# Performance work log

Hardware: AMD Instinct MI355X
Metric: run time of the kernel (lower is better)

Reference implementation:

```python
import jax, jax.numpy as jnp
import numpy as np

D_HEAD = 64
D_MODEL = 1024
N_HEADS = D_MODEL // D_HEAD
MAX_TOKENS = 2048


def setup_inputs() -> dict:
    key = jax.random.key(0)
    ks = jax.random.split(key, 5)
    batch, pos = 2, 2048
    # kaiming_normal_ on (n_heads, d_model, d_head): fan_in = d_model*d_head -> std = sqrt(2/fan_in)
    std_qkv = np.sqrt(2.0 / (D_MODEL * D_HEAD)).astype(np.float32)
    # xavier_normal_ on (d_model, d_model): std = sqrt(2/(fan_in+fan_out))
    std_out = np.sqrt(2.0 / (D_MODEL + D_MODEL)).astype(np.float32)
    return {
        "residual_stream": jax.random.normal(ks[0], (batch, pos, D_MODEL), dtype=jnp.float32),
        "weight_query": jax.random.normal(ks[1], (N_HEADS, D_MODEL, D_HEAD), dtype=jnp.float32) * std_qkv,
        "weight_key": jax.random.normal(ks[2], (N_HEADS, D_MODEL, D_HEAD), dtype=jnp.float32) * std_qkv,
        "weight_value": jax.random.normal(ks[3], (N_HEADS, D_MODEL, D_HEAD), dtype=jnp.float32) * std_qkv,
        "weight_out": jax.random.normal(ks[4], (D_MODEL, D_MODEL), dtype=jnp.float32) * std_out,
    }


def reference(residual_stream, weight_query, weight_key, weight_value, weight_out):
    # QKV projections: [b, p, m] x [h, m, d] -> [b, h, p, d]
    q = jnp.einsum('bpm,hmd->bhpd', residual_stream, weight_query)
    k = jnp.einsum('bpm,hmd->bhpd', residual_stream, weight_key)
    v = jnp.einsum('bpm,hmd->bhpd', residual_stream, weight_value)

    n_tokens = residual_stream.shape[1]
    # scaled scores [b, h, dest, src]
    scores = jnp.einsum('bhqd,bhkd->bhqk', q, k) / jnp.sqrt(jnp.float32(D_HEAD))
    # causal mask: -inf above the diagonal
    causal = jnp.tril(jnp.ones((n_tokens, n_tokens), dtype=bool))
    scores = jnp.where(causal, scores, jnp.float32(-jnp.inf))
    pattern = jax.nn.softmax(scores, axis=-1)

    attn = jnp.einsum('bhqk,bhkd->bhqd', pattern, v)  # [b, h, dest, d_head]
    # concat heads -> [b, p, h*d_head]
    b, h, p, d = attn.shape
    attn_concat = jnp.transpose(attn, (0, 2, 1, 3)).reshape(b, p, h * d)
    return jnp.einsum('bpm,mn->bpn', attn_concat, weight_out)
```

## Files before the change

kernel.cpp:

```cpp
#include <hip/hip_runtime.h>
#include <hip/hip_bf16.h>
#include <stdint.h>


typedef __bf16 bf16x8 __attribute__((ext_vector_type(8)));
typedef float f32x4 __attribute__((ext_vector_type(4)));
typedef float f32x16 __attribute__((ext_vector_type(16)));
typedef unsigned short u16;

__device__ __forceinline__ u16 f2bf(float f) {
  unsigned u = __float_as_uint(f);
  u += 0x7fffu + ((u >> 16) & 1u);
  return (u16)(u >> 16);
}

__device__ __forceinline__ uint32_t cvtpk(float lo, float hi) {
  uint32_t r;
  asm("v_cvt_pk_bf16_f32 %0, %1, %2" : "=v"(r) : "v"(lo), "v"(hi));
  return r;
}

__device__ __forceinline__ void pl32swap(uint32_t& a, uint32_t& b) {
  asm volatile("v_permlane32_swap_b32 %0, %1" : "+v"(a), "+v"(b));
}

__device__ __forceinline__ void gload16(const u16* g, u16* l) {
  __builtin_amdgcn_global_load_lds(
      (__attribute__((address_space(1))) void*)(g),
      (__attribute__((address_space(3))) void*)(l), 16, 0, 0);
}

__global__ __launch_bounds__(256) void prep_k(const float* __restrict__ X,
                                              const float* __restrict__ Wq,
                                              const float* __restrict__ Wk,
                                              const float* __restrict__ Wv,
                                              const float* __restrict__ Wo,
                                              u16* __restrict__ Xb,
                                              u16* __restrict__ WqT,
                                              u16* __restrict__ WoT) {
  __shared__ u16 tile[64][80];
  int bid = blockIdx.x, t = threadIdx.x;

  if (bid < 2048) {
    int i = (bid * 256 + t) * 8;
    float4 f0 = *reinterpret_cast<const float4*>(X + i);
    float4 f1 = *reinterpret_cast<const float4*>(X + i + 4);
    u16 tmp[8] = {f2bf(f0.x), f2bf(f0.y), f2bf(f0.z), f2bf(f0.w),
                  f2bf(f1.x), f2bf(f1.y), f2bf(f1.z), f2bf(f1.w)};
    *reinterpret_cast<uint4*>(Xb + i) = *reinterpret_cast<uint4*>(tmp);
    return;
  }

  const float* ip;
  u16* op;
  int r0, C, R;
  if (bid < 2816) {
    int tq = bid - 2048;
    int rb = tq & 15, z = tq >> 4;
    int sel = z >> 4, head = z & 15;
    const float* W = (sel == 0) ? Wq : (sel == 1 ? Wk : Wv);
    ip = W + (size_t)head * 65536;
    op = WqT + (size_t)sel * 1048576 + (size_t)head * 65536;
    r0 = rb * 64;
    C = 64;
    R = 1024;
    int r = t >> 2, cb = (t & 3) * 16;
    const float4* src = reinterpret_cast<const float4*>(ip + (size_t)(r0 + r) * C + cb);
    u16 tmp[16];
#pragma unroll
    for (int v = 0; v < 4; v++) {
      float4 f = src[v];
      tmp[v * 4 + 0] = f2bf(f.x);
      tmp[v * 4 + 1] = f2bf(f.y);
      tmp[v * 4 + 2] = f2bf(f.z);
      tmp[v * 4 + 3] = f2bf(f.w);
    }
    *reinterpret_cast<uint4*>(&tile[r][cb]) = *reinterpret_cast<uint4*>(&tmp[0]);
    *reinterpret_cast<uint4*>(&tile[r][cb + 8]) = *reinterpret_cast<uint4*>(&tmp[8]);
    __syncthreads();
    int c = t >> 2, rbq = (t & 3) * 16;
    uint4 outv[2];
    u16* tp = reinterpret_cast<u16*>(outv);
#pragma unroll
    for (int j = 0; j < 16; j++) tp[j] = tile[rbq + j][c];
    uint4* dst = reinterpret_cast<uint4*>(op + (size_t)c * R + r0 + rbq);
    dst[0] = outv[0];
    dst[1] = outv[1];
    return;
  }

  {
    int tc = bid - 2816;
    r0 = (tc & 15) * 64;
    int c0 = (tc >> 4) * 64;
    C = 1024; R = 1024;
    ip = Wo;
    op = WoT;
    int r = t >> 2, cb = (t & 3) * 16;
    const float4* src = reinterpret_cast<const float4*>(ip + (size_t)(r0 + r) * C + c0 + cb);
    u16 tmp[16];
#pragma unroll
    for (int v = 0; v < 4; v++) {
      float4 f = src[v];
      tmp[v * 4 + 0] = f2bf(f.x);
      tmp[v * 4 + 1] = f2bf(f.y);
      tmp[v * 4 + 2] = f2bf(f.z);
      tmp[v * 4 + 3] = f2bf(f.w);
    }
    *reinterpret_cast<uint4*>(&tile[r][cb]) = *reinterpret_cast<uint4*>(&tmp[0]);
    *reinterpret_cast<uint4*>(&tile[r][cb + 8]) = *reinterpret_cast<uint4*>(&tmp[8]);
    __syncthreads();
    int c = t >> 2, rbq = (t & 3) * 16;
    uint4 outv[2];
    u16* tp = reinterpret_cast<u16*>(outv);
#pragma unroll
    for (int j = 0; j < 16; j++) tp[j] = tile[rbq + j][c];
    uint4* dst = reinterpret_cast<uint4*>(op + (size_t)(c0 + c) * R + r0 + rbq);
    dst[0] = outv[0];
    dst[1] = outv[1];
  }
}

__device__ __forceinline__ void gemm128_core(const u16* __restrict__ A,
                                             const u16* __restrict__ BT,
                                             int m0, int n0,
                                             f32x4 (&acc)[4][4]) {
  __shared__ __align__(16) u16 As[2][128][64];
  __shared__ __align__(16) u16 Bs[2][128][64];
  int t = threadIdx.x, l = t & 63;
  int w = t >> 6, wm = w & 1, wn = w >> 1;
  int l15 = l & 15, q4 = l >> 4;
  int r8 = l >> 3;
  int cs = ((l & 7) ^ r8) * 8;
  int swz = l15 & 7;
  int srow = w * 32 + r8;
  const u16* ga = A + (size_t)(m0 + srow) * 1024 + cs;
  const u16* gb = BT + (size_t)(n0 + srow) * 1024 + cs;
  f32x4 z4 = {0.f, 0.f, 0.f, 0.f};
#pragma unroll
  for (int mi = 0; mi < 4; mi++)
#pragma unroll
    for (int nt = 0; nt < 4; nt++) acc[mi][nt] = z4;

#pragma unroll
  for (int i = 0; i < 4; i++) {
    gload16(ga + (size_t)(i * 8) * 1024, &As[0][w * 32 + i * 8][0]);
    gload16(gb + (size_t)(i * 8) * 1024, &Bs[0][w * 32 + i * 8][0]);
  }
  __syncthreads();

  for (int step = 0; step < 16; step++) {
    int cur = step & 1;
    if (step < 15) {
      int k0 = (step + 1) * 64;
#pragma unroll
      for (int i = 0; i < 4; i++) {
        gload16(ga + (size_t)(i * 8) * 1024 + k0, &As[cur ^ 1][w * 32 + i * 8][0]);
        gload16(gb + (size_t)(i * 8) * 1024 + k0, &Bs[cur ^ 1][w * 32 + i * 8][0]);
      }
    }
#pragma unroll
    for (int kk = 0; kk < 2; kk++) {
      bf16x8 af[4], bfr[4];
#pragma unroll
      for (int mi = 0; mi < 4; mi++)
        af[mi] = *reinterpret_cast<const bf16x8*>(
            &As[cur][wm * 64 + mi * 16 + l15][((kk * 4 + q4) ^ swz) * 8]);
#pragma unroll
      for (int nt = 0; nt < 4; nt++)
        bfr[nt] = *reinterpret_cast<const bf16x8*>(
            &Bs[cur][wn * 64 + nt * 16 + l15][((kk * 4 + q4) ^ swz) * 8]);
#pragma unroll
      for (int mi = 0; mi < 4; mi++)
#pragma unroll
        for (int nt = 0; nt < 4; nt++)
          acc[mi][nt] = __builtin_amdgcn_mfma_f32_16x16x32_bf16(af[mi], bfr[nt], acc[mi][nt], 0, 0, 0);
    }
    __syncthreads();
  }
}

__global__ __launch_bounds__(256) void qkv_gemm128_k(const u16* __restrict__ A,
                                                     const u16* __restrict__ BT,
                                                     u16* __restrict__ Q,
                                                     u16* __restrict__ K,
                                                     u16* __restrict__ VT2) {
  __shared__ __align__(16) u16 As[2][128][32];
  __shared__ __align__(16) u16 Bs[2][128][32];
  const float QSCALE = 0.125f * 1.44269504088896340736f;
  int m0 = blockIdx.x * 128, n0 = blockIdx.y * 128;
  int t = threadIdx.x, l = t & 63;
  int w = t >> 6, wm = w & 1, wn = w >> 1;
  int l15 = l & 15, q4 = l >> 4;
  int g = ((l & 3) - (l >> 3)) & 3;
  size_t lsrc = (size_t)(l >> 2) * 1024 + (size_t)(g * 8);
  const u16* ga = A + (size_t)(m0 + w * 32) * 1024 + lsrc;
  const u16* gb = BT + (size_t)(n0 + w * 32) * 1024 + lsrc;
  int rch = ((q4 + (l15 >> 1)) & 3) * 8;

  f32x4 acc[4][4];
  f32x4 z4 = {0.f, 0.f, 0.f, 0.f};
#pragma unroll
  for (int mi = 0; mi < 4; mi++)
#pragma unroll
    for (int nt = 0; nt < 4; nt++) acc[mi][nt] = z4;

  auto stage = [&](int buf, int k0) {
    gload16(ga + k0, &As[buf][w * 32][0]);
    gload16(ga + (size_t)16 * 1024 + k0, &As[buf][w * 32 + 16][0]);
    gload16(gb + k0, &Bs[buf][w * 32][0]);
    gload16(gb + (size_t)16 * 1024 + k0, &Bs[buf][w * 32 + 16][0]);
  };

  stage(0, 0);
  __syncthreads();

  for (int step = 0; step < 32; step++) {
    int cur = step & 1;
    if (step < 31) stage(cur ^ 1, (step + 1) * 32);
    bf16x8 af[4], bfr[4];
#pragma unroll
    for (int mi = 0; mi < 4; mi++)
      af[mi] = *reinterpret_cast<const bf16x8*>(&As[cur][wm * 64 + mi * 16 + l15][rch]);
#pragma unroll
    for (int nt = 0; nt < 4; nt++)
      bfr[nt] = *reinterpret_cast<const bf16x8*>(&Bs[cur][wn * 64 + nt * 16 + l15][rch]);
    __builtin_amdgcn_s_setprio(1);
#pragma unroll
    for (int mi = 0; mi < 4; mi++)
#pragma unroll
      for (int nt = 0; nt < 4; nt++)
        acc[mi][nt] = __builtin_amdgcn_mfma_f32_16x16x32_bf16(af[mi], bfr[nt], acc[mi][nt], 0, 0, 0);
    __builtin_amdgcn_s_setprio(0);
    __syncthreads();
  }

#pragma unroll
  for (int mi = 0; mi < 4; mi++) {
#pragma unroll
    for (int nt = 0; nt < 4; nt++) {
#pragma unroll
      for (int r = 0; r < 4; r++) {
        int m = m0 + wm * 64 + mi * 16 + q4 * 4 + r;
        int n = n0 + wn * 64 + nt * 16 + l15;
        int wsel = n >> 10, h = (n >> 6) & 15, d = n & 63;
        int b = m >> 11, p = m & 2047;
        size_t bh = (size_t)(b * 16 + h);
        float v = acc[mi][nt][r];
        if (wsel == 0)
          Q[(bh * 2048 + p) * 64 + d] = f2bf(v * QSCALE);
        else if (wsel == 1)
          K[(bh * 2048 + p) * 64 + d] = f2bf(v);
        else
          VT2[((bh * 32 + (p >> 6)) * 64 + d) * 64 + (p & 63)] = f2bf(v);
      }
    }
  }
}

__global__ __launch_bounds__(256) void out_gemm128_k(const u16* __restrict__ A,
                                                     const u16* __restrict__ BT,
                                                     float* __restrict__ O) {
  int m0 = blockIdx.x * 128, n0 = blockIdx.y * 128;
  f32x4 acc[4][4];
  gemm128_core(A, BT, m0, n0, acc);
  int t = threadIdx.x, l = t & 63;
  int w = t >> 6, wm = w & 1, wn = w >> 1;
  int l15 = l & 15, q4 = l >> 4;
#pragma unroll
  for (int mi = 0; mi < 4; mi++) {
#pragma unroll
    for (int nt = 0; nt < 4; nt++) {
#pragma unroll
      for (int r = 0; r < 4; r++) {
        int m = m0 + wm * 64 + mi * 16 + q4 * 4 + r;
        int n = n0 + wn * 64 + nt * 16 + l15;
        O[(size_t)m * 1024 + n] = acc[mi][nt][r];
      }
    }
  }
}

__global__ __launch_bounds__(256) void attn_k(const u16* __restrict__ Q,
                                              const u16* __restrict__ K,
                                              const u16* __restrict__ VT2,
                                              u16* __restrict__ A) {
  __shared__ __align__(16) u16 Ks[2][64][64];
  __shared__ __align__(16) u16 Vs[2][64][64];
  int pr = blockIdx.x, h = blockIdx.y, b = blockIdx.z;
  int qt = b ? (15 - pr) : pr;
  size_t bh = (size_t)(b * 16 + h);
  const u16* Qp = Q + bh * 2048 * 64;
  const u16* Kp = K + bh * 2048 * 64;
  const u16* Vt = VT2 + bh * 32 * 64 * 64;
  int t = threadIdx.x, l = t & 63, w = t >> 6;
  int l31 = l & 31, hi = l >> 5;
  int r8 = l >> 3, cs = ((l & 7) ^ r8) * 8;
  int swz = l31 & 7;
  const float NEG = -1e30f;
  int nkt = 2 * qt + 2;
  const u16* kbase = Kp + (size_t)(w * 16 + r8) * 64 + cs;
  const u16* vbase = Vt + (size_t)(w * 16 + r8) * 64 + cs;
  int qrow = qt * 128 + w * 32 + l31;

  uint32_t onesw[4] = {0x3F803F80u, 0x3F803F80u, 0x3F803F80u, 0x3F803F80u};
  bf16x8 onesb = *reinterpret_cast<const bf16x8*>(onesw);

  bf16x8 qb[4];
#pragma unroll
  for (int kc = 0; kc < 4; kc++)
    qb[kc] = *reinterpret_cast<const bf16x8*>(Qp + (size_t)qrow * 64 + kc * 16 + hi * 8);

  f32x16 accO[2], rs_acc;
#pragma unroll
  for (int dh = 0; dh < 2; dh++)
#pragma unroll
    for (int r = 0; r < 16; r++) accO[dh][r] = 0.f;
#pragma unroll
  for (int r = 0; r < 16; r++) rs_acc[r] = 0.f;

#pragma unroll
  for (int j = 0; j < 2; j++) {
    gload16(kbase + (size_t)(j * 512), &Ks[0][w * 16 + j * 8][0]);
    gload16(vbase + (size_t)(j * 512), &Vs[0][w * 16 + j * 8][0]);
  }
  __syncthreads();

  for (int kt = 0; kt < nkt; kt++) {
    int cur = kt & 1;
    if (kt < nkt - 1) {
      size_t off = (size_t)(kt + 1) * 4096;
#pragma unroll
      for (int j = 0; j < 2; j++) {
        gload16(kbase + off + j * 512, &Ks[cur ^ 1][w * 16 + j * 8][0]);
        gload16(vbase + off + j * 512, &Vs[cur ^ 1][w * 16 + j * 8][0]);
      }
    }

    f32x16 st[2];
#pragma unroll
    for (int kvh = 0; kvh < 2; kvh++)
#pragma unroll
      for (int r = 0; r < 16; r++) st[kvh][r] = 0.f;
    __builtin_amdgcn_s_setprio(1);
#pragma unroll
    for (int kc = 0; kc < 4; kc++) {
      bf16x8 ka0 = *reinterpret_cast<const bf16x8*>(
          &Ks[cur][l31][((2 * kc + hi) ^ swz) * 8]);
      bf16x8 ka1 = *reinterpret_cast<const bf16x8*>(
          &Ks[cur][32 + l31][((2 * kc + hi) ^ swz) * 8]);
      st[0] = __builtin_amdgcn_mfma_f32_32x32x16_bf16(ka0, qb[kc], st[0], 0, 0, 0);
      st[1] = __builtin_amdgcn_mfma_f32_32x32x16_bf16(ka1, qb[kc], st[1], 0, 0, 0);
    }
    __builtin_amdgcn_s_setprio(0);

    if (kt >= 2 * qt) {
      int kvb = kt * 64;
#pragma unroll
      for (int kvh = 0; kvh < 2; kvh++)
#pragma unroll
        for (int r = 0; r < 16; r++) {
          int kv = kvb + kvh * 32 + (r & 3) + 8 * (r >> 2) + 4 * hi;
          if (kv > qrow) st[kvh][r] = NEG;
        }
    }

#pragma unroll
    for (int kvh = 0; kvh < 2; kvh++)
#pragma unroll
      for (int r = 0; r < 16; r++) st[kvh][r] = exp2f(st[kvh][r]);

    bf16x8 pa[4];
#pragma unroll
    for (int ks = 0; ks < 4; ks++) {
      const f32x16& pp = st[ks >> 1];
      const int s8 = (ks & 1) * 8;
      uint32_t x0 = cvtpk(pp[s8 + 0], pp[s8 + 1]);
      uint32_t x1 = cvtpk(pp[s8 + 2], pp[s8 + 3]);
      uint32_t y0 = cvtpk(pp[s8 + 4], pp[s8 + 5]);
      uint32_t y1 = cvtpk(pp[s8 + 6], pp[s8 + 7]);
      pl32swap(x0, y0);
      pl32swap(x1, y1);
      uint32_t wds[4] = {x0, x1, y0, y1};
      pa[ks] = *reinterpret_cast<const bf16x8*>(wds);
    }

    __builtin_amdgcn_s_setprio(1);
#pragma unroll
    for (int ks = 0; ks < 4; ks++)
      rs_acc = __builtin_amdgcn_mfma_f32_32x32x16_bf16(pa[ks], onesb, rs_acc, 0, 0, 0);
#pragma unroll
    for (int dh = 0; dh < 2; dh++)
#pragma unroll
      for (int ks = 0; ks < 4; ks++) {
        bf16x8 vb = *reinterpret_cast<const bf16x8*>(
            &Vs[cur][dh * 32 + l31][((2 * ks + hi) ^ swz) * 8]);
        accO[dh] = __builtin_amdgcn_mfma_f32_32x32x16_bf16(pa[ks], vb, accO[dh], 0, 0, 0);
      }
    __builtin_amdgcn_s_setprio(0);
    __syncthreads();
  }

#pragma unroll
  for (int r = 0; r < 16; r++) {
    float inv = 1.f / rs_acc[r];
    int ql = (r & 3) + 8 * (r >> 2) + 4 * hi;
    int prow = qt * 128 + w * 32 + ql;
    size_t base = ((size_t)(b * 2048 + prow)) * 1024 + h * 64;
    A[base + l31] = f2bf(accO[0][r] * inv);
    A[base + 32 + l31] = f2bf(accO[1][r] * inv);
  }
}

extern "C" void kernel_launch(void* const* d_in, const int* in_sizes, int n_in,
                              void* d_out, int out_size, void* d_ws, size_t ws_size,
                              hipStream_t stream) {
  const float* X  = (const float*)d_in[0];
  const float* Wq = (const float*)d_in[1];
  const float* Wk = (const float*)d_in[2];
  const float* Wv = (const float*)d_in[3];
  const float* Wo = (const float*)d_in[4];
  float* out = (float*)d_out;

  u16* ws = (u16*)d_ws;
  u16* WqT = ws;
  u16* WoT = WqT + 3145728;
  u16* Xb  = WoT + 1048576;
  u16* Qb  = Xb + 4194304;
  u16* Kb  = Qb + 4194304;
  u16* VT2 = Kb + 4194304;
  u16* Ab  = Xb;

  prep_k<<<dim3(3072), 256, 0, stream>>>(X, Wq, Wk, Wv, Wo, Xb, WqT, WoT);
  qkv_gemm128_k<<<dim3(32, 24), 256, 0, stream>>>(Xb, WqT, Qb, Kb, VT2);
  attn_k<<<dim3(16, 16, 2), 256, 0, stream>>>(Qb, Kb, VT2, Ab);
  out_gemm128_k<<<dim3(32, 8), 256, 0, stream>>>(Ab, WoT, out);
}
```

Baseline: 197.1 us.

## Split long causal attention tiles across blocks and retile output GEMM

The attention kernel now splits the KV range of the eight longest query tiles in two. One block writes partial O and row sums to a workspace and raises a flag; the other block spin-waits on that flag and merges the partials. This balances work across the causal triangle and raises the block count from 512 to 768. The output GEMM moves to 128x64 tiles with K-step 32, doubling its grid to 512 blocks for better occupancy, and exp2f is replaced by a raw v_exp_f32. The spin-wait depends on the producer block being scheduled, which risks deadlock or stalls, and the partial buffers add global memory traffic.

```diff
diff --git a/kernel.cpp b/kernel.cpp
--- a/kernel.cpp
+++ b/kernel.cpp
@@ -22,6 +22,12 @@
 
 __device__ __forceinline__ void pl32swap(uint32_t& a, uint32_t& b) {
   asm volatile("v_permlane32_swap_b32 %0, %1" : "+v"(a), "+v"(b));
+}
+
+__device__ __forceinline__ float fexp2(float x) {
+  float r;
+  asm("v_exp_f32 %0, %1" : "=v"(r) : "v"(x));
+  return r;
 }
 
 __device__ __forceinline__ void gload16(const u16* g, u16* l) {
@@ -37,9 +43,15 @@
                                               const float* __restrict__ Wo,
                                               u16* __restrict__ Xb,
                                               u16* __restrict__ WqT,
-                                              u16* __restrict__ WoT) {
+                                              u16* __restrict__ WoT,
+                                              int* __restrict__ flags) {
   __shared__ u16 tile[64][80];
   int bid = blockIdx.x, t = threadIdx.x;
+
+  if (bid == 3072) {
+    flags[t] = 0;
+    return;
+  }
 
   if (bid < 2048) {
     int i = (bid * 256 + t) * 8;
@@ -51,21 +63,16 @@
     return;
   }
 
-  const float* ip;
-  u16* op;
-  int r0, C, R;
   if (bid < 2816) {
     int tq = bid - 2048;
     int rb = tq & 15, z = tq >> 4;
     int sel = z >> 4, head = z & 15;
     const float* W = (sel == 0) ? Wq : (sel == 1 ? Wk : Wv);
-    ip = W + (size_t)head * 65536;
-    op = WqT + (size_t)sel * 1048576 + (size_t)head * 65536;
-    r0 = rb * 64;
-    C = 64;
-    R = 1024;
+    const float* ip = W + (size_t)head * 65536;
+    u16* op = WqT + (size_t)sel * 1048576 + (size_t)head * 65536;
+    int r0 = rb * 64;
     int r = t >> 2, cb = (t & 3) * 16;
-    const float4* src = reinterpret_cast<const float4*>(ip + (size_t)(r0 + r) * C + cb);
+    const float4* src = reinterpret_cast<const float4*>(ip + (size_t)(r0 + r) * 64 + cb);
     u16 tmp[16];
 #pragma unroll
     for (int v = 0; v < 4; v++) {
@@ -83,7 +90,7 @@
     u16* tp = reinterpret_cast<u16*>(outv);
 #pragma unroll
     for (int j = 0; j < 16; j++) tp[j] = tile[rbq + j][c];
-    uint4* dst = reinterpret_cast<uint4*>(op + (size_t)c * R + r0 + rbq);
+    uint4* dst = reinterpret_cast<uint4*>(op + (size_t)c * 1024 + r0 + rbq);
     dst[0] = outv[0];
     dst[1] = outv[1];
     return;
@@ -91,13 +98,10 @@
 
   {
     int tc = bid - 2816;
-    r0 = (tc & 15) * 64;
+    int r0 = (tc & 15) * 64;
     int c0 = (tc >> 4) * 64;
-    C = 1024; R = 1024;
-    ip = Wo;
-    op = WoT;
     int r = t >> 2, cb = (t & 3) * 16;
-    const float4* src = reinterpret_cast<const float4*>(ip + (size_t)(r0 + r) * C + c0 + cb);
+    const float4* src = reinterpret_cast<const float4*>(Wo + (size_t)(r0 + r) * 1024 + c0 + cb);
     u16 tmp[16];
 #pragma unroll
     for (int v = 0; v < 4; v++) {
@@ -115,68 +119,9 @@
     u16* tp = reinterpret_cast<u16*>(outv);
 #pragma unroll
     for (int j = 0; j < 16; j++) tp[j] = tile[rbq + j][c];
-    uint4* dst = reinterpret_cast<uint4*>(op + (size_t)(c0 + c) * R + r0 + rbq);
+    uint4* dst = reinterpret_cast<uint4*>(WoT + (size_t)(c0 + c) * 1024 + r0 + rbq);
     dst[0] = outv[0];
     dst[1] = outv[1];
-  }
-}
-
-__device__ __forceinline__ void gemm128_core(const u16* __restrict__ A,
-                                             const u16* __restrict__ BT,
-                                             int m0, int n0,
-                                             f32x4 (&acc)[4][4]) {
-  __shared__ __align__(16) u16 As[2][128][64];
-  __shared__ __align__(16) u16 Bs[2][128][64];
-  int t = threadIdx.x, l = t & 63;
-  int w = t >> 6, wm = w & 1, wn = w >> 1;
-  int l15 = l & 15, q4 = l >> 4;
-  int r8 = l >> 3;
-  int cs = ((l & 7) ^ r8) * 8;
-  int swz = l15 & 7;
-  int srow = w * 32 + r8;
-  const u16* ga = A + (size_t)(m0 + srow) * 1024 + cs;
-  const u16* gb = BT + (size_t)(n0 + srow) * 1024 + cs;
-  f32x4 z4 = {0.f, 0.f, 0.f, 0.f};
-#pragma unroll
-  for (int mi = 0; mi < 4; mi++)
-#pragma unroll
-    for (int nt = 0; nt < 4; nt++) acc[mi][nt] = z4;
-
-#pragma unroll
-  for (int i = 0; i < 4; i++) {
-    gload16(ga + (size_t)(i * 8) * 1024, &As[0][w * 32 + i * 8][0]);
-    gload16(gb + (size_t)(i * 8) * 1024, &Bs[0][w * 32 + i * 8][0]);
-  }
-  __syncthreads();
-
-  for (int step = 0; step < 16; step++) {
-    int cur = step & 1;
-    if (step < 15) {
-      int k0 = (step + 1) * 64;
-#pragma unroll
-      for (int i = 0; i < 4; i++) {
-        gload16(ga + (size_t)(i * 8) * 1024 + k0, &As[cur ^ 1][w * 32 + i * 8][0]);
-        gload16(gb + (size_t)(i * 8) * 1024 + k0, &Bs[cur ^ 1][w * 32 + i * 8][0]);
-      }
-    }
-#pragma unroll
-    for (int kk = 0; kk < 2; kk++) {
-      bf16x8 af[4], bfr[4];
-#pragma unroll
-      for (int mi = 0; mi < 4; mi++)
-        af[mi] = *reinterpret_cast<const bf16x8*>(
-            &As[cur][wm * 64 + mi * 16 + l15][((kk * 4 + q4) ^ swz) * 8]);
-#pragma unroll
-      for (int nt = 0; nt < 4; nt++)
-        bfr[nt] = *reinterpret_cast<const bf16x8*>(
-            &Bs[cur][wn * 64 + nt * 16 + l15][((kk * 4 + q4) ^ swz) * 8]);
-#pragma unroll
-      for (int mi = 0; mi < 4; mi++)
-#pragma unroll
-        for (int nt = 0; nt < 4; nt++)
-          acc[mi][nt] = __builtin_amdgcn_mfma_f32_16x16x32_bf16(af[mi], bfr[nt], acc[mi][nt], 0, 0, 0);
-    }
-    __syncthreads();
   }
 }
 
@@ -258,23 +203,65 @@
   }
 }
 
-__global__ __launch_bounds__(256) void out_gemm128_k(const u16* __restrict__ A,
-                                                     const u16* __restrict__ BT,
-                                                     float* __restrict__ O) {
-  int m0 = blockIdx.x * 128, n0 = blockIdx.y * 128;
-  f32x4 acc[4][4];
-  gemm128_core(A, BT, m0, n0, acc);
+__global__ __launch_bounds__(256) void out_gemm64_k(const u16* __restrict__ A,
+                                                    const u16* __restrict__ BT,
+                                                    float* __restrict__ O) {
+  __shared__ __align__(16) u16 As[2][128][32];
+  __shared__ __align__(16) u16 Bs[2][64][32];
+  int m0 = blockIdx.x * 128, n0 = blockIdx.y * 64;
   int t = threadIdx.x, l = t & 63;
-  int w = t >> 6, wm = w & 1, wn = w >> 1;
+  int w = t >> 6, wm = w >> 1, wn = w & 1;
   int l15 = l & 15, q4 = l >> 4;
+  int g = ((l & 3) - (l >> 3)) & 3;
+  size_t lsrc = (size_t)(l >> 2) * 1024 + (size_t)(g * 8);
+  const u16* ga = A + (size_t)(m0 + w * 32) * 1024 + lsrc;
+  const u16* gb = BT + (size_t)(n0 + w * 16) * 1024 + lsrc;
+  int rch = ((q4 + (l15 >> 1)) & 3) * 8;
+
+  f32x4 acc[4][2];
+  f32x4 z4 = {0.f, 0.f, 0.f, 0.f};
+#pragma unroll
+  for (int mi = 0; mi < 4; mi++)
+#pragma unroll
+    for (int nt = 0; nt < 2; nt++) acc[mi][nt] = z4;
+
+  auto stage = [&](int buf, int k0) {
+    gload16(ga + k0, &As[buf][w * 32][0]);
+    gload16(ga + (size_t)16 * 1024 + k0, &As[buf][w * 32 + 16][0]);
+    gload16(gb + k0, &Bs[buf][w * 16][0]);
+  };
+
+  stage(0, 0);
+  __syncthreads();
+
+  for (int step = 0; step < 32; step++) {
+    int cur = step & 1;
+    if (step < 31) stage(cur ^ 1, (step + 1) * 32);
+    bf16x8 af[4], bfr[2];
+#pragma unroll
+    for (int mi = 0; mi < 4; mi++)
+      af[mi] = *reinterpret_cast<const bf16x8*>(&As[cur][wm * 64 + mi * 16 + l15][rch]);
+#pragma unroll
+    for (int nt = 0; nt < 2; nt++)
+      bfr[nt] = *reinterpret_cast<const bf16x8*>(&Bs[cur][wn * 32 + nt * 16 + l15][rch]);
+    __builtin_amdgcn_s_setprio(1);
+#pragma unroll
+    for (int mi = 0; mi < 4; mi++)
+#pragma unroll
+      for (int nt = 0; nt < 2; nt++)
+        acc[mi][nt] = __builtin_amdgcn_mfma_f32_16x16x32_bf16(af[mi], bfr[nt], acc[mi][nt], 0, 0, 0);
+    __builtin_amdgcn_s_setprio(0);
+    __syncthreads();
+  }
+
 #pragma unroll
   for (int mi = 0; mi < 4; mi++) {
 #pragma unroll
-    for (int nt = 0; nt < 4; nt++) {
+    for (int nt = 0; nt < 2; nt++) {
 #pragma unroll
       for (int r = 0; r < 4; r++) {
         int m = m0 + wm * 64 + mi * 16 + q4 * 4 + r;
-        int n = n0 + wn * 64 + nt * 16 + l15;
+        int n = n0 + wn * 32 + nt * 16 + l15;
         O[(size_t)m * 1024 + n] = acc[mi][nt][r];
       }
     }
@@ -284,12 +271,19 @@
 __global__ __launch_bounds__(256) void attn_k(const u16* __restrict__ Q,
                                               const u16* __restrict__ K,
                                               const u16* __restrict__ VT2,
-                                              u16* __restrict__ A) {
+                                              u16* __restrict__ A,
+                                              float* __restrict__ Opart,
+                                              int* __restrict__ flags) {
   __shared__ __align__(16) u16 Ks[2][64][64];
   __shared__ __align__(16) u16 Vs[2][64][64];
-  int pr = blockIdx.x, h = blockIdx.y, b = blockIdx.z;
-  int qt = b ? (15 - pr) : pr;
+  int jx = blockIdx.x, h = blockIdx.y, b = blockIdx.z;
+  int qt, ktA, ktB;
+  bool wrHalf = false, cmHalf = false;
+  if (jx < 8)       { qt = jx;      ktA = 0;      ktB = 2 * qt + 2; }
+  else if (jx < 16) { qt = 23 - jx; ktA = 0;      ktB = qt + 1;  wrHalf = true; }
+  else              { qt = 31 - jx; ktA = qt + 1; ktB = 2 * qt + 2; cmHalf = true; }
   size_t bh = (size_t)(b * 16 + h);
+  int ps = (int)bh * 8 + (qt - 8);
   const u16* Qp = Q + bh * 2048 * 64;
   const u16* Kp = K + bh * 2048 * 64;
   const u16* Vt = VT2 + bh * 32 * 64 * 64;
@@ -298,7 +292,6 @@
   int r8 = l >> 3, cs = ((l & 7) ^ r8) * 8;
   int swz = l31 & 7;
   const float NEG = -1e30f;
-  int nkt = 2 * qt + 2;
   const u16* kbase = Kp + (size_t)(w * 16 + r8) * 64 + cs;
   const u16* vbase = Vt + (size_t)(w * 16 + r8) * 64 + cs;
   int qrow = qt * 128 + w * 32 + l31;
@@ -321,14 +314,14 @@
 
 #pragma unroll
   for (int j = 0; j < 2; j++) {
-    gload16(kbase + (size_t)(j * 512), &Ks[0][w * 16 + j * 8][0]);
-    gload16(vbase + (size_t)(j * 512), &Vs[0][w * 16 + j * 8][0]);
+    gload16(kbase + (size_t)ktA * 4096 + j * 512, &Ks[ktA & 1][w * 16 + j * 8][0]);
+    gload16(vbase + (size_t)ktA * 4096 + j * 512, &Vs[ktA & 1][w * 16 + j * 8][0]);
   }
   __syncthreads();
 
-  for (int kt = 0; kt < nkt; kt++) {
+  for (int kt = ktA; kt < ktB; kt++) {
     int cur = kt & 1;
-    if (kt < nkt - 1) {
+    if (kt < ktB - 1) {
       size_t off = (size_t)(kt + 1) * 4096;
 #pragma unroll
       for (int j = 0; j < 2; j++) {
@@ -368,7 +361,7 @@
 #pragma unroll
     for (int kvh = 0; kvh < 2; kvh++)
 #pragma unroll
-      for (int r = 0; r < 16; r++) st[kvh][r] = exp2f(st[kvh][r]);
+      for (int r = 0; r < 16; r++) st[kvh][r] = fexp2(st[kvh][r]);
 
     bf16x8 pa[4];
 #pragma unroll
@@ -401,6 +394,35 @@
     __syncthreads();
   }
 
+  if (wrHalf) {
+    float* op = Opart + (size_t)ps * 12288;
+#pragma unroll
+    for (int i = 0; i < 16; i++) op[i * 256 + t] = accO[0][i];
+#pragma unroll
+    for (int i = 0; i < 16; i++) op[(16 + i) * 256 + t] = accO[1][i];
+#pragma unroll
+    for (int i = 0; i < 16; i++) op[(32 + i) * 256 + t] = rs_acc[i];
+    __threadfence();
+    __syncthreads();
+    if (t == 0)
+      __hip_atomic_store(&flags[ps], 1, __ATOMIC_RELEASE, __HIP_MEMORY_SCOPE_AGENT);
+    return;
+  }
+  if (cmHalf) {
+    if (t == 0) {
+      while (__hip_atomic_load(&flags[ps], __ATOMIC_ACQUIRE, __HIP_MEMORY_SCOPE_AGENT) == 0)
+        __builtin_amdgcn_s_sleep(8);
+    }
+    __syncthreads();
+    const float* op = Opart + (size_t)ps * 12288;
+#pragma unroll
+    for (int i = 0; i < 16; i++) accO[0][i] += op[i * 256 + t];
+#pragma unroll
+    for (int i = 0; i < 16; i++) accO[1][i] += op[(16 + i) * 256 + t];
+#pragma unroll
+    for (int i = 0; i < 16; i++) rs_acc[i] += op[(32 + i) * 256 + t];
+  }
+
 #pragma unroll
   for (int r = 0; r < 16; r++) {
     float inv = 1.f / rs_acc[r];
@@ -430,9 +452,11 @@
   u16* Kb  = Qb + 4194304;
   u16* VT2 = Kb + 4194304;
   u16* Ab  = Xb;
-
-  prep_k<<<dim3(3072), 256, 0, stream>>>(X, Wq, Wk, Wv, Wo, Xb, WqT, WoT);
+  float* Opart = (float*)(VT2 + 4194304);
+  int* flags = (int*)(Opart + 3145728);
+
+  prep_k<<<dim3(3073), 256, 0, stream>>>(X, Wq, Wk, Wv, Wo, Xb, WqT, WoT, flags);
   qkv_gemm128_k<<<dim3(32, 24), 256, 0, stream>>>(Xb, WqT, Qb, Kb, VT2);
-  attn_k<<<dim3(16, 16, 2), 256, 0, stream>>>(Qb, Kb, VT2, Ab);
-  out_gemm128_k<<<dim3(32, 8), 256, 0, stream>>>(Ab, WoT, out);
-}
+  attn_k<<<dim3(24, 16, 2), 256, 0, stream>>>(Qb, Kb, VT2, Ab, Opart, flags);
+  out_gemm64_k<<<dim3(32, 16), 256, 0, stream>>>(Ab, WoT, out);
+}
```

Result: slower. 222.6 us (+12.9%).
